# Optimization experiments

Measured on AMD Instinct MI355X. Metric: run time of the kernel, lower is better.

Reference implementation:

```python
import jax, jax.numpy as jnp
import numpy as np
from jax.scipy.special import logsumexp

D, E, V = 512, 4, 32000
B, L = 1, 1024


def setup_inputs() -> dict:
    key = jax.random.key(0)
    ks = jax.random.split(key, 5)
    s = 0.02
    return {
        "hidden_states": jax.random.normal(ks[0], (B, L, D), dtype=jnp.float32),
        "W_prior": jax.random.normal(ks[1], (D, E), dtype=jnp.float32) * s,
        "b_prior": jnp.zeros((E,), dtype=jnp.float32),
        "W_latent": jax.random.normal(ks[2], (D, E * D), dtype=jnp.float32) * s,
        "b_latent": jnp.zeros((E * D,), dtype=jnp.float32),
        "W_dec": jax.random.normal(ks[3], (D, V), dtype=jnp.float32) * s,
        "b_dec": jnp.zeros((V,), dtype=jnp.float32),
    }


def reference(hidden_states, W_prior, b_prior, W_latent, b_latent, W_dec, b_dec):
    # hidden_states: [B, L, D]
    b, l, d = hidden_states.shape
    e = W_prior.shape[1]
    # mixture coefficients (split_hidden=False path): softmax over experts
    mix_logits = hidden_states @ W_prior + b_prior                 # [B, L, E]
    log_coef = jax.nn.log_softmax(mix_logits, axis=-1)             # [B, L, E]
    # per-expert latent projections with tanh
    latent = jnp.tanh(hidden_states @ W_latent + b_latent)         # [B, L, E*D]
    latent = latent.reshape(b, l, e, d)                            # [B, L, E, D]
    # shared decoder to vocab
    logits = jnp.einsum("bled,dv->blev", latent, W_dec) + b_dec    # [B, L, E, V]
    logp = jax.nn.log_softmax(logits, axis=-1)                     # [B, L, E, V]
    # log(sum_e coef_e * softmax_e) == logsumexp_e(log_coef_e + log_softmax_e)
    out = logsumexp(logp + log_coef[..., None], axis=2)            # [B, L, V]
    return out
```

## Files before the change

kernel.cpp:

```cpp
#include <hip/hip_runtime.h>
#include <hip/hip_bf16.h>
#include <hip/hip_fp16.h>
#include <math.h>


#define D_ 512
#define E_ 4
#define V_ 32000
#define L_ 1024
#define AROWS (L_ * E_)

#define SA_ 0x7D7D7D7D
#define SB_ 0x7B7B7B7B

typedef __attribute__((ext_vector_type(8))) short s16x8;
typedef __attribute__((ext_vector_type(4))) float f32x4;
typedef __attribute__((ext_vector_type(2))) float f32x2;
typedef __attribute__((ext_vector_type(4))) int i32x4;
typedef __attribute__((ext_vector_type(8))) int i32x8;
typedef __attribute__((ext_vector_type(4))) unsigned int u32x4;
typedef const __attribute__((address_space(1))) char* gp1_t;
typedef __attribute__((address_space(3))) char* lp3_t;

__device__ __forceinline__ void gload_lds16(const void* g, void* l) {
  __builtin_amdgcn_global_load_lds((gp1_t)g, (lp3_t)l, 16, 0, 0);
}

#define PREP_DEC  8000
#define PREP_LAT  (PREP_DEC + 1024)
#define PREP_CVT  (PREP_LAT + 512)
#define PREP_PRI  (PREP_CVT + 256)
#define PREP_TOT  (PREP_PRI + 16)

__global__ __launch_bounds__(256) void prep_kernel(
    const float* __restrict__ hs, const float* __restrict__ W_prior,
    const float* __restrict__ b_prior, const float* __restrict__ W_latent,
    const float* __restrict__ W_dec,
    __hip_bfloat16* __restrict__ hs_bf, __hip_bfloat16* __restrict__ WlatT,
    unsigned char* __restrict__ WdecT8, float* __restrict__ log_coef,
    float* __restrict__ S) {
  __shared__ float tileS[64 * 33];
  const int b = blockIdx.x;
  const int tid = threadIdx.x;

  if (b < PREP_DEC) {
    const int vb = (b % 1000) * 32;
    const int db = (b / 1000) * 64;
    {
      const int r = tid >> 2, c0 = (tid & 3) * 8;
      const float* src = W_dec + (size_t)(db + r) * V_ + vb + c0;
      float4 a0 = *(const float4*)src;
      float4 a1 = *(const float4*)(src + 4);
      float* t = &tileS[r * 33 + c0];
      t[0] = a0.x; t[1] = a0.y; t[2] = a0.z; t[3] = a0.w;
      t[4] = a1.x; t[5] = a1.y; t[6] = a1.z; t[7] = a1.w;
    }
    __syncthreads();
    {
      const int vr = tid >> 3, d0 = (tid & 7) * 8;
      float t8[8];
      #pragma unroll
      for (int j = 0; j < 8; ++j) t8[j] = tileS[(d0 + j) * 33 + vr] * 16.f;
      unsigned int u0 = 0, u1 = 0;
      u0 = __builtin_amdgcn_cvt_pk_fp8_f32(t8[0], t8[1], u0, false);
      u0 = __builtin_amdgcn_cvt_pk_fp8_f32(t8[2], t8[3], u0, true);
      u1 = __builtin_amdgcn_cvt_pk_fp8_f32(t8[4], t8[5], u1, false);
      u1 = __builtin_amdgcn_cvt_pk_fp8_f32(t8[6], t8[7], u1, true);
      uint2 uu = {u0, u1};
      *(uint2*)&WdecT8[(size_t)(vb + vr) * D_ + db + d0] = uu;
    }
  } else if (b < PREP_LAT) {
    const int bb = b - PREP_DEC;
    const int cb = (bb & 63) * 32, rb = (bb >> 6) * 32;
    const int C = E_ * D_, R = D_;
    const int tx = tid & 31, ty = tid >> 5;
    #pragma unroll
    for (int j = 0; j < 32; j += 8)
      tileS[(ty + j) * 33 + tx] = W_latent[(size_t)(rb + ty + j) * C + cb + tx];
    __syncthreads();
    #pragma unroll
    for (int j = 0; j < 32; j += 8)
      WlatT[(size_t)(cb + ty + j) * R + rb + tx] = __float2bfloat16(tileS[tx * 33 + ty + j]);
  } else if (b < PREP_CVT) {
    int i = ((b - PREP_LAT) * 256 + tid) * 4;
    float4 v = *(const float4*)(hs + i);
    hs_bf[i + 0] = __float2bfloat16(v.x);
    hs_bf[i + 1] = __float2bfloat16(v.y);
    hs_bf[i + 2] = __float2bfloat16(v.z);
    hs_bf[i + 3] = __float2bfloat16(v.w);
  } else if (b < PREP_PRI) {
    int t = (b - PREP_CVT) * 4 + (tid >> 6);
    int lane = tid & 63;
    float a0 = 0.f, a1 = 0.f, a2 = 0.f, a3 = 0.f;
    for (int d = lane; d < D_; d += 64) {
      float h = hs[t * D_ + d];
      float4 w = ((const float4*)W_prior)[d];
      a0 += h * w.x; a1 += h * w.y; a2 += h * w.z; a3 += h * w.w;
    }
    #pragma unroll
    for (int off = 32; off > 0; off >>= 1) {
      a0 += __shfl_xor(a0, off);
      a1 += __shfl_xor(a1, off);
      a2 += __shfl_xor(a2, off);
      a3 += __shfl_xor(a3, off);
    }
    a0 += b_prior[0]; a1 += b_prior[1]; a2 += b_prior[2]; a3 += b_prior[3];
    float mx = fmaxf(fmaxf(a0, a1), fmaxf(a2, a3));
    float ls = mx + logf(expf(a0 - mx) + expf(a1 - mx) + expf(a2 - mx) + expf(a3 - mx));
    if (lane == 0) {
      log_coef[t * 4 + 0] = a0 - ls;
      log_coef[t * 4 + 1] = a1 - ls;
      log_coef[t * 4 + 2] = a2 - ls;
      log_coef[t * 4 + 3] = a3 - ls;
    }
  } else {
    S[(b - PREP_PRI) * 256 + tid] = 0.f;
  }
}

__global__ void qk_kernel(const float* __restrict__ log_coef, const float* __restrict__ S,
                          float* __restrict__ q) {
  int i = blockIdx.x * blockDim.x + threadIdx.x;
  if (i < AROWS) q[i] = __expf(log_coef[i]) / S[i];
}

__global__ __launch_bounds__(256, 2) void latent_gemm(
    const __hip_bfloat16* __restrict__ Abf, const __hip_bfloat16* __restrict__ BT,
    const float* __restrict__ b_latent, unsigned char* __restrict__ latent8) {
  __shared__ short As[128 * 32];
  __shared__ short Bs[128 * 32];
  const int tid = threadIdx.x;
  const int wave = tid >> 6, lane = tid & 63;
  const int wm = wave >> 1, wn = wave & 1;
  const int m0 = blockIdx.y * 128;
  const int n0 = blockIdx.x * 128;
  const int lrow = lane & 15;
  const int kgrp = lane >> 4;
  const int srow = wave * 16 + (lane >> 2);
  const int scol = (lane & 3) * 8;

  f32x4 acc[4][4];
  #pragma unroll
  for (int mt = 0; mt < 4; ++mt)
    #pragma unroll
    for (int nt = 0; nt < 4; ++nt) acc[mt][nt] = f32x4{0.f, 0.f, 0.f, 0.f};

  for (int kt = 0; kt < 16; ++kt) {
    const int k0 = kt * 32;
    #pragma unroll
    for (int j = 0; j < 2; ++j) {
      const int row = j * 64 + srow;
      gload_lds16(Abf + (size_t)(m0 + row) * D_ + k0 + scol, &As[(j * 256 + wave * 64) * 8]);
      gload_lds16(BT + (size_t)(n0 + row) * D_ + k0 + scol, &Bs[(j * 256 + wave * 64) * 8]);
    }
    __syncthreads();
    s16x8 af[4], bfr[4];
    #pragma unroll
    for (int mt = 0; mt < 4; ++mt) af[mt] = *(const s16x8*)&As[(wm * 64 + mt * 16 + lrow) * 32 + kgrp * 8];
    #pragma unroll
    for (int nt = 0; nt < 4; ++nt) bfr[nt] = *(const s16x8*)&Bs[(wn * 64 + nt * 16 + lrow) * 32 + kgrp * 8];
    #pragma unroll
    for (int mt = 0; mt < 4; ++mt)
      #pragma unroll
      for (int nt = 0; nt < 4; ++nt)
        acc[mt][nt] = __builtin_amdgcn_mfma_f32_16x16x32_bf16(af[mt], bfr[nt], acc[mt][nt], 0, 0, 0);
    __syncthreads();
  }

  float blat[4];
  #pragma unroll
  for (int nt = 0; nt < 4; ++nt) blat[nt] = b_latent[n0 + wn * 64 + nt * 16 + lrow];
  #pragma unroll
  for (int mt = 0; mt < 4; ++mt)
    #pragma unroll
    for (int r = 0; r < 4; ++r) {
      const int row = m0 + wm * 64 + mt * 16 + kgrp * 4 + r;
      #pragma unroll
      for (int nt = 0; nt < 4; ++nt) {
        const int col = n0 + wn * 64 + nt * 16 + lrow;
        float v = tanhf(acc[mt][nt][r] + blat[nt]) * 4.f;
        int u = __builtin_amdgcn_cvt_pk_fp8_f32(v, v, 0, false);
        latent8[(size_t)row * (E_ * D_) + col] = (unsigned char)(u & 0xff);
      }
    }
}

template <int MODE>
__global__ __launch_bounds__(256, 2) void mos_gemm(
    const unsigned char* __restrict__ A8,
    const unsigned char* __restrict__ W8,
    const float* __restrict__ b_dec,
    const float* __restrict__ q,
    float* __restrict__ S,
    float* __restrict__ out,
    unsigned int* __restrict__ pbuf) {
  const int bid = blockIdx.x;
  const int xcd = bid & 7;
  const int idx = bid >> 3;
  const int mg = xcd >> 2;
  const int vg = xcd & 3;
  const int vt = vg * 63 + (idx >> 4);
  const int mtile = mg * 16 + (idx & 15);
  if (vt >= V_ / 128) return;
  const int m0 = mtile * 128;
  const int v0 = vt * 128;

  __shared__ __attribute__((aligned(16))) unsigned char As[128 * 128];
  __shared__ __attribute__((aligned(16))) unsigned char Bs[128 * 128];
  const int tid = threadIdx.x;
  const int wave = tid >> 6, lane = tid & 63;
  const int wm = wave >> 1, wn = wave & 1;
  const int lrow = lane & 15;
  const int kgrp = lane >> 4;
  const int srow8 = wave * 8 + (lane >> 3);
  const int schunk = lane & 7;

  float bdec[4];
  #pragma unroll
  for (int nt = 0; nt < 4; ++nt) bdec[nt] = b_dec[v0 + wn * 64 + nt * 16 + lrow];

  f32x4 acc[4][4];
  #pragma unroll
  for (int mt = 0; mt < 4; ++mt)
    #pragma unroll
    for (int nt = 0; nt < 4; ++nt) acc[mt][nt] = f32x4{0.f, 0.f, 0.f, 0.f};

  for (int kt = 0; kt < 4; ++kt) {
    const int kb = kt * 128;
    #pragma unroll
    for (int j = 0; j < 4; ++j) {
      const int row = j * 32 + srow8;
      const int sc = (schunk ^ (row & 7)) * 16;
      gload_lds16(A8 + (size_t)(m0 + row) * D_ + kb + sc, &As[(j * 32 + wave * 8) * 128]);
      gload_lds16(W8 + (size_t)(v0 + row) * D_ + kb + sc, &Bs[(j * 32 + wave * 8) * 128]);
    }
    __syncthreads();
    i32x8 af[4], bfr[4];
    #pragma unroll
    for (int mt = 0; mt < 4; ++mt) {
      const int row = wm * 64 + mt * 16 + lrow;
      const int s = lrow & 7;
      i32x4 lo = *(const i32x4*)&As[row * 128 + (((kgrp * 2) ^ s) * 16)];
      i32x4 hi = *(const i32x4*)&As[row * 128 + (((kgrp * 2 + 1) ^ s) * 16)];
      af[mt] = __builtin_shufflevector(lo, hi, 0, 1, 2, 3, 4, 5, 6, 7);
    }
    #pragma unroll
    for (int nt = 0; nt < 4; ++nt) {
      const int row = wn * 64 + nt * 16 + lrow;
      const int s = lrow & 7;
      i32x4 lo = *(const i32x4*)&Bs[row * 128 + (((kgrp * 2) ^ s) * 16)];
      i32x4 hi = *(const i32x4*)&Bs[row * 128 + (((kgrp * 2 + 1) ^ s) * 16)];
      bfr[nt] = __builtin_shufflevector(lo, hi, 0, 1, 2, 3, 4, 5, 6, 7);
    }
    #pragma unroll
    for (int mt = 0; mt < 4; ++mt)
      #pragma unroll
      for (int nt = 0; nt < 4; ++nt)
        acc[mt][nt] = __builtin_amdgcn_mfma_scale_f32_16x16x128_f8f6f4(
            af[mt], bfr[nt], acc[mt][nt], 0, 0, 0, SA_, 0, SB_);
    __syncthreads();
  }

  if constexpr (MODE == 1 || MODE == 3) {
    #pragma unroll
    for (int mt = 0; mt < 4; ++mt) {
      const int row4 = m0 + wm * 64 + mt * 16 + kgrp * 4;
      const int token = row4 >> 2;
      float p0 = 0.f, p1 = 0.f, p2 = 0.f, p3 = 0.f;
      #pragma unroll
      for (int nt = 0; nt < 4; ++nt) {
        float e0 = __expf(acc[mt][nt][0] + bdec[nt]);
        float e1 = __expf(acc[mt][nt][1] + bdec[nt]);
        float e2 = __expf(acc[mt][nt][2] + bdec[nt]);
        float e3 = __expf(acc[mt][nt][3] + bdec[nt]);
        p0 += e0; p1 += e1; p2 += e2; p3 += e3;
        if constexpr (MODE == 3) {
          const int v = v0 + wn * 64 + nt * 16 + lrow;
          int u = 0;
          u = __builtin_amdgcn_cvt_pk_fp8_f32(e0, e1, u, false);
          u = __builtin_amdgcn_cvt_pk_fp8_f32(e2, e3, u, true);
          __builtin_nontemporal_store((unsigned int)u, &pbuf[(size_t)token * V_ + v]);
        }
      }
      #pragma unroll
      for (int off = 1; off < 16; off <<= 1) {
        p0 += __shfl_xor(p0, off);
        p1 += __shfl_xor(p1, off);
        p2 += __shfl_xor(p2, off);
        p3 += __shfl_xor(p3, off);
      }
      if (lrow == 0) {
        atomicAdd(&S[row4 + 0], p0);
        atomicAdd(&S[row4 + 1], p1);
        atomicAdd(&S[row4 + 2], p2);
        atomicAdd(&S[row4 + 3], p3);
      }
    }
  } else {
    #pragma unroll
    for (int mt = 0; mt < 4; ++mt) {
      const int row4 = m0 + wm * 64 + mt * 16 + kgrp * 4;
      const float4 qv = *(const float4*)&q[row4];
      const int token = row4 >> 2;
      #pragma unroll
      for (int nt = 0; nt < 4; ++nt) {
        float v = qv.x * __expf(acc[mt][nt][0] + bdec[nt]) +
                  qv.y * __expf(acc[mt][nt][1] + bdec[nt]) +
                  qv.z * __expf(acc[mt][nt][2] + bdec[nt]) +
                  qv.w * __expf(acc[mt][nt][3] + bdec[nt]);
        out[(size_t)token * V_ + v0 + wn * 64 + nt * 16 + lrow] = __logf(v);
      }
    }
  }
}

__global__ __launch_bounds__(256) void combine_kernel(
    const unsigned int* __restrict__ pbuf,
    const float* __restrict__ lc, const float* __restrict__ S,
    float* __restrict__ out) {
  const int t = blockIdx.y;
  const int v = blockIdx.x * 1024 + threadIdx.x * 4;
  if (v >= V_) return;
  const float4 lcv = ((const float4*)lc)[t];
  const float4 Sv = ((const float4*)S)[t];
  const float q0 = __expf(lcv.x) / Sv.x;
  const float q1 = __expf(lcv.y) / Sv.y;
  const float q2 = __expf(lcv.z) / Sv.z;
  const float q3 = __expf(lcv.w) / Sv.w;
  u32x4 u = __builtin_nontemporal_load((const u32x4*)(pbuf + (size_t)t * V_ + v));
  float4 o;
  #pragma unroll
  for (int j = 0; j < 4; ++j) {
    unsigned int w = u[j];
    f32x2 lo = __builtin_amdgcn_cvt_pk_f32_fp8(w, false);
    f32x2 hi = __builtin_amdgcn_cvt_pk_f32_fp8(w, true);
    float s = q0 * lo.x + q1 * lo.y + q2 * hi.x + q3 * hi.y;
    ((float*)&o)[j] = __logf(s);
  }
  *(float4*)&out[(size_t)t * V_ + v] = o;
}

extern "C" void kernel_launch(void* const* d_in, const int* in_sizes, int n_in,
                              void* d_out, int out_size, void* d_ws, size_t ws_size,
                              hipStream_t stream) {
  const float* hs       = (const float*)d_in[0];
  const float* W_prior  = (const float*)d_in[1];
  const float* b_prior  = (const float*)d_in[2];
  const float* W_latent = (const float*)d_in[3];
  const float* b_latent = (const float*)d_in[4];
  const float* W_dec    = (const float*)d_in[5];
  const float* b_dec    = (const float*)d_in[6];
  float* out = (float*)d_out;

  char* ws = (char*)d_ws;
  __hip_bfloat16* hs_bf   = (__hip_bfloat16*)(ws);
  __hip_bfloat16* WlatT   = (__hip_bfloat16*)(ws + (1u << 20));
  unsigned char*  latent8 = (unsigned char*)(ws + 3u * (1u << 20));
  unsigned char*  WdecT8  = (unsigned char*)(ws + 5u * (1u << 20));
  float* log_coef = (float*)(ws + 22u * (1u << 20));
  float* S = log_coef + AROWS;
  float* q = S + AROWS;
  unsigned int* pbuf = (unsigned int*)(ws + 23u * (1u << 20));

  const size_t needA = 23u * (1u << 20) + (size_t)L_ * V_ * 4;
  const bool pathA = ws_size >= needA;

  prep_kernel<<<PREP_TOT, 256, 0, stream>>>(hs, W_prior, b_prior, W_latent, W_dec,
                                            hs_bf, WlatT, WdecT8, log_coef, S);
  latent_gemm<<<dim3((E_ * D_) / 128, L_ / 128), 256, 0, stream>>>(hs_bf, WlatT, b_latent, latent8);

  if (pathA) {
    mos_gemm<3><<<8 * 16 * 63, 256, 0, stream>>>(latent8, WdecT8, b_dec, nullptr, S, nullptr, pbuf);
    combine_kernel<<<dim3(32, L_), 256, 0, stream>>>(pbuf, log_coef, S, out);
  } else {
    mos_gemm<1><<<8 * 16 * 63, 256, 0, stream>>>(latent8, WdecT8, b_dec, nullptr, S, nullptr, nullptr);
    qk_kernel<<<(AROWS + 255) / 256, 256, 0, stream>>>(log_coef, S, q);
    mos_gemm<2><<<8 * 16 * 63, 256, 0, stream>>>(latent8, WdecT8, b_dec, q, nullptr, out, nullptr);
  }
}
```

Baseline: 357.9 us.

## Widen prep tiles, halve latent GEMM N-tile, DPP reductions, loop combine kernel

The prep kernel now transposes 64x64 tiles with wider vector stores for W_dec fp8, W_latent bf16 and the hidden-state conversion, so it launches fewer blocks and issues wider memory transactions. The latent GEMM N-tile drops from 128 to 64, doubling its grid, and mos_gemm asks for three blocks per SIMD instead of two. The row-of-16 reductions in mos_gemm use DPP row shifts instead of xor shuffles, with the result now read from lane 15. The combine kernel uses 2 blocks per token that each loop over half a row instead of 32 single-pass blocks. The occupancy hint may force register spills in mos_gemm, and the smaller latent tiles reuse loaded data less.

Measured after the change: 380.6 us. 6.4% more time.

```diff
diff --git a/kernel.cpp b/kernel.cpp
--- a/kernel.cpp
+++ b/kernel.cpp
@@ -26,9 +26,22 @@
   __builtin_amdgcn_global_load_lds((gp1_t)g, (lp3_t)l, 16, 0, 0);
 }
 
-#define PREP_DEC  8000
-#define PREP_LAT  (PREP_DEC + 1024)
-#define PREP_CVT  (PREP_LAT + 512)
+__device__ __forceinline__ float dpp_row16_sum(float x) {
+  int t;
+  t = __builtin_amdgcn_update_dpp(0, __float_as_int(x), 0x111, 0xF, 0xF, true);
+  x += __int_as_float(t);
+  t = __builtin_amdgcn_update_dpp(0, __float_as_int(x), 0x112, 0xF, 0xF, true);
+  x += __int_as_float(t);
+  t = __builtin_amdgcn_update_dpp(0, __float_as_int(x), 0x114, 0xF, 0xF, true);
+  x += __int_as_float(t);
+  t = __builtin_amdgcn_update_dpp(0, __float_as_int(x), 0x118, 0xF, 0xF, true);
+  x += __int_as_float(t);
+  return x;
+}
+
+#define PREP_DEC  4000
+#define PREP_LAT  (PREP_DEC + 256)
+#define PREP_CVT  (PREP_LAT + 256)
 #define PREP_PRI  (PREP_CVT + 256)
 #define PREP_TOT  (PREP_PRI + 16)
 
@@ -39,55 +52,74 @@
     __hip_bfloat16* __restrict__ hs_bf, __hip_bfloat16* __restrict__ WlatT,
     unsigned char* __restrict__ WdecT8, float* __restrict__ log_coef,
     float* __restrict__ S) {
-  __shared__ float tileS[64 * 33];
+  __shared__ float tileS[64 * 65];
   const int b = blockIdx.x;
   const int tid = threadIdx.x;
 
   if (b < PREP_DEC) {
-    const int vb = (b % 1000) * 32;
-    const int db = (b / 1000) * 64;
+    const int vb = (b % 500) * 64;
+    const int db = (b / 500) * 64;
     {
-      const int r = tid >> 2, c0 = (tid & 3) * 8;
+      const int r = tid >> 2, c0 = (tid & 3) * 16;
       const float* src = W_dec + (size_t)(db + r) * V_ + vb + c0;
-      float4 a0 = *(const float4*)src;
-      float4 a1 = *(const float4*)(src + 4);
-      float* t = &tileS[r * 33 + c0];
-      t[0] = a0.x; t[1] = a0.y; t[2] = a0.z; t[3] = a0.w;
-      t[4] = a1.x; t[5] = a1.y; t[6] = a1.z; t[7] = a1.w;
+      float* t = &tileS[r * 65 + c0];
+      #pragma unroll
+      for (int j = 0; j < 4; ++j) {
+        float4 a = *(const float4*)(src + j * 4);
+        t[j * 4 + 0] = a.x; t[j * 4 + 1] = a.y; t[j * 4 + 2] = a.z; t[j * 4 + 3] = a.w;
+      }
     }
     __syncthreads();
     {
-      const int vr = tid >> 3, d0 = (tid & 7) * 8;
-      float t8[8];
-      #pragma unroll
-      for (int j = 0; j < 8; ++j) t8[j] = tileS[(d0 + j) * 33 + vr] * 16.f;
-      unsigned int u0 = 0, u1 = 0;
-      u0 = __builtin_amdgcn_cvt_pk_fp8_f32(t8[0], t8[1], u0, false);
-      u0 = __builtin_amdgcn_cvt_pk_fp8_f32(t8[2], t8[3], u0, true);
-      u1 = __builtin_amdgcn_cvt_pk_fp8_f32(t8[4], t8[5], u1, false);
-      u1 = __builtin_amdgcn_cvt_pk_fp8_f32(t8[6], t8[7], u1, true);
-      uint2 uu = {u0, u1};
-      *(uint2*)&WdecT8[(size_t)(vb + vr) * D_ + db + d0] = uu;
+      const int vr = tid >> 2, d0 = (tid & 3) * 16;
+      float t16[16];
+      #pragma unroll
+      for (int j = 0; j < 16; ++j) t16[j] = tileS[(d0 + j) * 65 + vr] * 16.f;
+      unsigned int u[4];
+      #pragma unroll
+      for (int j = 0; j < 4; ++j) {
+        unsigned int w = 0;
+        w = __builtin_amdgcn_cvt_pk_fp8_f32(t16[j * 4 + 0], t16[j * 4 + 1], w, false);
+        w = __builtin_amdgcn_cvt_pk_fp8_f32(t16[j * 4 + 2], t16[j * 4 + 3], w, true);
+        u[j] = w;
+      }
+      u32x4 uu = {u[0], u[1], u[2], u[3]};
+      *(u32x4*)&WdecT8[(size_t)(vb + vr) * D_ + db + d0] = uu;
     }
   } else if (b < PREP_LAT) {
     const int bb = b - PREP_DEC;
-    const int cb = (bb & 63) * 32, rb = (bb >> 6) * 32;
-    const int C = E_ * D_, R = D_;
-    const int tx = tid & 31, ty = tid >> 5;
-    #pragma unroll
-    for (int j = 0; j < 32; j += 8)
-      tileS[(ty + j) * 33 + tx] = W_latent[(size_t)(rb + ty + j) * C + cb + tx];
-    __syncthreads();
-    #pragma unroll
-    for (int j = 0; j < 32; j += 8)
-      WlatT[(size_t)(cb + ty + j) * R + rb + tx] = __float2bfloat16(tileS[tx * 33 + ty + j]);
+    const int cb = (bb & 31) * 64, rb = (bb >> 5) * 64;
+    const int C = E_ * D_;
+    {
+      const int r = tid >> 2, c0 = (tid & 3) * 16;
+      const float* src = W_latent + (size_t)(rb + r) * C + cb + c0;
+      float* t = &tileS[r * 65 + c0];
+      #pragma unroll
+      for (int j = 0; j < 4; ++j) {
+        float4 a = *(const float4*)(src + j * 4);
+        t[j * 4 + 0] = a.x; t[j * 4 + 1] = a.y; t[j * 4 + 2] = a.z; t[j * 4 + 3] = a.w;
+      }
+    }
+    __syncthreads();
+    {
+      const int cr = tid >> 2, r0 = (tid & 3) * 16;
+      __hip_bfloat16 tmp[16];
+      #pragma unroll
+      for (int j = 0; j < 16; ++j) tmp[j] = __float2bfloat16(tileS[(r0 + j) * 65 + cr]);
+      __hip_bfloat16* dst = &WlatT[(size_t)(cb + cr) * D_ + rb + r0];
+      *(uint4*)dst = *(uint4*)&tmp[0];
+      *(uint4*)(dst + 8) = *(uint4*)&tmp[8];
+    }
   } else if (b < PREP_CVT) {
-    int i = ((b - PREP_LAT) * 256 + tid) * 4;
-    float4 v = *(const float4*)(hs + i);
-    hs_bf[i + 0] = __float2bfloat16(v.x);
-    hs_bf[i + 1] = __float2bfloat16(v.y);
-    hs_bf[i + 2] = __float2bfloat16(v.z);
-    hs_bf[i + 3] = __float2bfloat16(v.w);
+    int i = ((b - PREP_LAT) * 256 + tid) * 8;
+    float4 v0 = *(const float4*)(hs + i);
+    float4 v1 = *(const float4*)(hs + i + 4);
+    __hip_bfloat16 tmp[8];
+    tmp[0] = __float2bfloat16(v0.x); tmp[1] = __float2bfloat16(v0.y);
+    tmp[2] = __float2bfloat16(v0.z); tmp[3] = __float2bfloat16(v0.w);
+    tmp[4] = __float2bfloat16(v1.x); tmp[5] = __float2bfloat16(v1.y);
+    tmp[6] = __float2bfloat16(v1.z); tmp[7] = __float2bfloat16(v1.w);
+    *(uint4*)&hs_bf[i] = *(uint4*)&tmp[0];
   } else if (b < PREP_PRI) {
     int t = (b - PREP_CVT) * 4 + (tid >> 6);
     int lane = tid & 63;
@@ -128,22 +160,22 @@
     const __hip_bfloat16* __restrict__ Abf, const __hip_bfloat16* __restrict__ BT,
     const float* __restrict__ b_latent, unsigned char* __restrict__ latent8) {
   __shared__ short As[128 * 32];
-  __shared__ short Bs[128 * 32];
+  __shared__ short Bs[64 * 32];
   const int tid = threadIdx.x;
   const int wave = tid >> 6, lane = tid & 63;
   const int wm = wave >> 1, wn = wave & 1;
   const int m0 = blockIdx.y * 128;
-  const int n0 = blockIdx.x * 128;
+  const int n0 = blockIdx.x * 64;
   const int lrow = lane & 15;
   const int kgrp = lane >> 4;
   const int srow = wave * 16 + (lane >> 2);
   const int scol = (lane & 3) * 8;
 
-  f32x4 acc[4][4];
+  f32x4 acc[4][2];
   #pragma unroll
   for (int mt = 0; mt < 4; ++mt)
     #pragma unroll
-    for (int nt = 0; nt < 4; ++nt) acc[mt][nt] = f32x4{0.f, 0.f, 0.f, 0.f};
+    for (int nt = 0; nt < 2; ++nt) acc[mt][nt] = f32x4{0.f, 0.f, 0.f, 0.f};
 
   for (int kt = 0; kt < 16; ++kt) {
     const int k0 = kt * 32;
@@ -151,33 +183,33 @@
     for (int j = 0; j < 2; ++j) {
       const int row = j * 64 + srow;
       gload_lds16(Abf + (size_t)(m0 + row) * D_ + k0 + scol, &As[(j * 256 + wave * 64) * 8]);
-      gload_lds16(BT + (size_t)(n0 + row) * D_ + k0 + scol, &Bs[(j * 256 + wave * 64) * 8]);
-    }
-    __syncthreads();
-    s16x8 af[4], bfr[4];
+    }
+    gload_lds16(BT + (size_t)(n0 + srow) * D_ + k0 + scol, &Bs[(wave * 64) * 8]);
+    __syncthreads();
+    s16x8 af[4], bfr[2];
     #pragma unroll
     for (int mt = 0; mt < 4; ++mt) af[mt] = *(const s16x8*)&As[(wm * 64 + mt * 16 + lrow) * 32 + kgrp * 8];
     #pragma unroll
-    for (int nt = 0; nt < 4; ++nt) bfr[nt] = *(const s16x8*)&Bs[(wn * 64 + nt * 16 + lrow) * 32 + kgrp * 8];
+    for (int nt = 0; nt < 2; ++nt) bfr[nt] = *(const s16x8*)&Bs[(wn * 32 + nt * 16 + lrow) * 32 + kgrp * 8];
     #pragma unroll
     for (int mt = 0; mt < 4; ++mt)
       #pragma unroll
-      for (int nt = 0; nt < 4; ++nt)
+      for (int nt = 0; nt < 2; ++nt)
         acc[mt][nt] = __builtin_amdgcn_mfma_f32_16x16x32_bf16(af[mt], bfr[nt], acc[mt][nt], 0, 0, 0);
     __syncthreads();
   }
 
-  float blat[4];
+  float blat[2];
   #pragma unroll
-  for (int nt = 0; nt < 4; ++nt) blat[nt] = b_latent[n0 + wn * 64 + nt * 16 + lrow];
+  for (int nt = 0; nt < 2; ++nt) blat[nt] = b_latent[n0 + wn * 32 + nt * 16 + lrow];
   #pragma unroll
   for (int mt = 0; mt < 4; ++mt)
     #pragma unroll
     for (int r = 0; r < 4; ++r) {
       const int row = m0 + wm * 64 + mt * 16 + kgrp * 4 + r;
       #pragma unroll
-      for (int nt = 0; nt < 4; ++nt) {
-        const int col = n0 + wn * 64 + nt * 16 + lrow;
+      for (int nt = 0; nt < 2; ++nt) {
+        const int col = n0 + wn * 32 + nt * 16 + lrow;
         float v = tanhf(acc[mt][nt][r] + blat[nt]) * 4.f;
         int u = __builtin_amdgcn_cvt_pk_fp8_f32(v, v, 0, false);
         latent8[(size_t)row * (E_ * D_) + col] = (unsigned char)(u & 0xff);
@@ -186,7 +218,7 @@
 }
 
 template <int MODE>
-__global__ __launch_bounds__(256, 2) void mos_gemm(
+__global__ __launch_bounds__(256, 3) void mos_gemm(
     const unsigned char* __restrict__ A8,
     const unsigned char* __restrict__ W8,
     const float* __restrict__ b_dec,
@@ -282,14 +314,11 @@
           __builtin_nontemporal_store((unsigned int)u, &pbuf[(size_t)token * V_ + v]);
         }
       }
-      #pragma unroll
-      for (int off = 1; off < 16; off <<= 1) {
-        p0 += __shfl_xor(p0, off);
-        p1 += __shfl_xor(p1, off);
-        p2 += __shfl_xor(p2, off);
-        p3 += __shfl_xor(p3, off);
-      }
-      if (lrow == 0) {
+      p0 = dpp_row16_sum(p0);
+      p1 = dpp_row16_sum(p1);
+      p2 = dpp_row16_sum(p2);
+      p3 = dpp_row16_sum(p3);
+      if (lrow == 15) {
         atomicAdd(&S[row4 + 0], p0);
         atomicAdd(&S[row4 + 1], p1);
         atomicAdd(&S[row4 + 2], p2);
@@ -319,25 +348,29 @@
     const float* __restrict__ lc, const float* __restrict__ S,
     float* __restrict__ out) {
   const int t = blockIdx.y;
-  const int v = blockIdx.x * 1024 + threadIdx.x * 4;
-  if (v >= V_) return;
+  const int vbase = blockIdx.x * (V_ / 2);
+  const int vend = vbase + (V_ / 2);
   const float4 lcv = ((const float4*)lc)[t];
   const float4 Sv = ((const float4*)S)[t];
   const float q0 = __expf(lcv.x) / Sv.x;
   const float q1 = __expf(lcv.y) / Sv.y;
   const float q2 = __expf(lcv.z) / Sv.z;
   const float q3 = __expf(lcv.w) / Sv.w;
-  u32x4 u = __builtin_nontemporal_load((const u32x4*)(pbuf + (size_t)t * V_ + v));
-  float4 o;
-  #pragma unroll
-  for (int j = 0; j < 4; ++j) {
-    unsigned int w = u[j];
-    f32x2 lo = __builtin_amdgcn_cvt_pk_f32_fp8(w, false);
-    f32x2 hi = __builtin_amdgcn_cvt_pk_f32_fp8(w, true);
-    float s = q0 * lo.x + q1 * lo.y + q2 * hi.x + q3 * hi.y;
-    ((float*)&o)[j] = __logf(s);
-  }
-  *(float4*)&out[(size_t)t * V_ + v] = o;
+  const unsigned int* prow = pbuf + (size_t)t * V_;
+  float* orow = out + (size_t)t * V_;
+  for (int v = vbase + threadIdx.x * 4; v < vend; v += 1024) {
+    u32x4 u = __builtin_nontemporal_load((const u32x4*)(prow + v));
+    float4 o;
+    #pragma unroll
+    for (int j = 0; j < 4; ++j) {
+      unsigned int w = u[j];
+      f32x2 lo = __builtin_amdgcn_cvt_pk_f32_fp8(w, false);
+      f32x2 hi = __builtin_amdgcn_cvt_pk_f32_fp8(w, true);
+      float s = q0 * lo.x + q1 * lo.y + q2 * hi.x + q3 * hi.y;
+      ((float*)&o)[j] = __logf(s);
+    }
+    *(float4*)(orow + v) = o;
+  }
 }
 
 extern "C" void kernel_launch(void* const* d_in, const int* in_sizes, int n_in,
@@ -367,11 +400,11 @@
 
   prep_kernel<<<PREP_TOT, 256, 0, stream>>>(hs, W_prior, b_prior, W_latent, W_dec,
                                             hs_bf, WlatT, WdecT8, log_coef, S);
-  latent_gemm<<<dim3((E_ * D_) / 128, L_ / 128), 256, 0, stream>>>(hs_bf, WlatT, b_latent, latent8);
+  latent_gemm<<<dim3((E_ * D_) / 64, L_ / 128), 256, 0, stream>>>(hs_bf, WlatT, b_latent, latent8);
 
   if (pathA) {
     mos_gemm<3><<<8 * 16 * 63, 256, 0, stream>>>(latent8, WdecT8, b_dec, nullptr, S, nullptr, pbuf);
-    combine_kernel<<<dim3(32, L_), 256, 0, stream>>>(pbuf, log_coef, S, out);
+    combine_kernel<<<dim3(2, L_), 256, 0, stream>>>(pbuf, log_coef, S, out);
   } else {
     mos_gemm<1><<<8 * 16 * 63, 256, 0, stream>>>(latent8, WdecT8, b_dec, nullptr, S, nullptr, nullptr);
     qk_kernel<<<(AROWS + 255) / 256, 256, 0, stream>>>(log_coef, S, q);
```
